# Kernel tuning notes

Hardware: AMD Instinct MI355X
Metric: run time of the kernel (lower is better)

Reference implementation:

```python
import jax, jax.numpy as jnp
import numpy as np

N_ACTOR = 128
NUM_MODS = 6
NUM_PTS = 30
N = 32768
B = 64
EPS = 1e-5


def _gn(x, g, b):
    # torch GroupNorm(1, C) on [..., C]: normalize over channel axis, affine
    m = jnp.mean(x, axis=-1, keepdims=True)
    v = jnp.mean((x - m) ** 2, axis=-1, keepdims=True)
    return (x - m) * jax.lax.rsqrt(v + EPS) * g + b


def setup_inputs() -> dict:
    key = jax.random.key(0)
    ks = jax.random.split(key, 32)
    d = N_ACTOR
    M = NUM_MODS
    s = 0.05
    rn = lambda k, shp: jax.random.normal(k, shp, jnp.float32) * s
    inp = {
        'actors': jax.random.normal(ks[0], (N, d), jnp.float32),
        'actor_ctrs': jax.random.normal(ks[1], (N, 2), jnp.float32),
        'actor_idcs': jnp.arange(N, dtype=jnp.int32).reshape(B, N // B),
        # per-mode residual MLP + output linear (stacked over modes)
        'pred_W1': rn(ks[2], (M, d, d)),
        'pred_g1': jnp.ones((M, d), jnp.float32),
        'pred_b1': jnp.zeros((M, d), jnp.float32),
        'pred_W2': rn(ks[3], (M, d, d)),
        'pred_g2': jnp.ones((M, d), jnp.float32),
        'pred_b2': jnp.zeros((M, d), jnp.float32),
        'pred_Wo': rn(ks[4], (M, d, 2 * NUM_PTS)),
        'pred_bo': rn(ks[5], (M, 2 * NUM_PTS)),
        # cls head: residual MLP + Linear(d,1)
        'cls_W1': rn(ks[6], (d, d)),
        'cls_g1': jnp.ones((d,), jnp.float32),
        'cls_b1': jnp.zeros((d,), jnp.float32),
        'cls_W2': rn(ks[7], (d, d)),
        'cls_g2': jnp.ones((d,), jnp.float32),
        'cls_b2': jnp.zeros((d,), jnp.float32),
        'cls_Wo': rn(ks[8], (d, 1)),
        'cls_bo': rn(ks[9], (1,)),
        # AttDest
        'att_dW1': rn(ks[10], (2, d)),
        'att_db1': rn(ks[11], (d,)),
        'att_dW2': rn(ks[12], (d, d)),
        'att_dg2': jnp.ones((d,), jnp.float32),
        'att_db2': jnp.zeros((d,), jnp.float32),
        'att_aW': rn(ks[13], (2 * d, d)),
        'att_ag': jnp.ones((d,), jnp.float32),
        'att_ab': jnp.zeros((d,), jnp.float32),
    }
    return inp


def reference(actors, actor_ctrs, actor_idcs, pred_W1, pred_g1, pred_b1,
              pred_W2, pred_g2, pred_b2, pred_Wo, pred_bo,
              cls_W1, cls_g1, cls_b1, cls_W2, cls_g2, cls_b2, cls_Wo, cls_bo,
              att_dW1, att_db1, att_dW2, att_dg2, att_db2,
              att_aW, att_ag, att_ab):
    n = actors.shape[0]
    M = pred_W1.shape[0]
    h = jnp.einsum('nc,mcd->mnd', actors, pred_W1)              # [M,N,d]
    h = jax.nn.relu(_gn(h, pred_g1[:, None, :], pred_b1[:, None, :]))
    h = _gn(jnp.einsum('mnd,mde->mne', h, pred_W2),
            pred_g2[:, None, :], pred_b2[:, None, :])
    h = jax.nn.relu(h + actors[None])                           # residual
    preds = jnp.einsum('mnd,mdo->mno', h, pred_Wo) + pred_bo[:, None, :]
    reg = preds.transpose(1, 0, 2).reshape(n, M, NUM_PTS, 2)    # [N,M,T,2]
    # per-scene reg[idcs] += ctrs: actor_idcs partitions arange(N), so this
    # is exactly a per-actor broadcast add of the (concatenated) centers
    reg = reg + actor_ctrs[:, None, None, :]
    dest_ctrs = jax.lax.stop_gradient(reg[:, :, -1, :])         # .detach()
    # --- AttDest ---
    dist = (actor_ctrs[:, None, :] - dest_ctrs).reshape(-1, 2)  # [N*M,2]
    dist = jax.nn.relu(dist @ att_dW1 + att_db1)
    dist = jax.nn.relu(_gn(dist @ att_dW2, att_dg2, att_db2))
    agts = jnp.broadcast_to(actors[:, None, :], (n, M, actors.shape[1]))
    agts = agts.reshape(-1, actors.shape[1])
    feats = jax.nn.relu(_gn(jnp.concatenate([dist, agts], axis=1) @ att_aW,
                            att_ag, att_ab))                    # [N*M,d]
    # --- cls head ---
    c = jax.nn.relu(_gn(feats @ cls_W1, cls_g1, cls_b1))
    c = _gn(c @ cls_W2, cls_g2, cls_b2)
    c = jax.nn.relu(c + feats)
    cls = (c @ cls_Wo + cls_bo).reshape(n, M)
    # --- sort modes by descending score, reorder reg accordingly ---
    order = jnp.argsort(-cls, axis=1)
    cls = jnp.take_along_axis(cls, order, axis=1)
    reg = jnp.take_along_axis(reg, order[:, :, None, None], axis=1)
    # train_model=True concatenates the per-scene splits back in order,
    # which reproduces the full arrays
    return cls, reg
```

## Files before the change

kernel.cpp:

```cpp
#include <hip/hip_runtime.h>

#define EPSV 1e-5f
#define CLS_SZ (32768*6)
#define FWS_FLOATS ((size_t)196608 * 128)

#define AL(ch,row) (((ch)<<7) + ((row) ^ ((((ch)&15))<<3)))

__device__ __forceinline__ float4 ld4(const float* p) { return *reinterpret_cast<const float4*>(p); }
__device__ __forceinline__ void st4(float* p, float4 v) { *reinterpret_cast<float4*>(p) = v; }

__device__ __forceinline__ void gemmA(const float* X, const float* __restrict__ Wg,
                                      float* WB0, float* WB1, float (&acc)[8][8],
                                      int ag, int jg4, int tid)
{
  float4 rA = ld4(Wg + tid*4);
  float4 rB = ld4(Wg + 1024 + tid*4);
  __syncthreads();
  st4(WB0 + tid*4, rA);
  st4(WB1 + tid*4, rB);
  __syncthreads();
  #pragma unroll 1
  for (int c = 0; c < 16; ++c) {
    float4 rN;
    const bool pf = (c + 2 < 16);
    if (pf) rN = ld4(Wg + (c+2)*1024 + tid*4);
    const float* WB = (c & 1) ? WB1 : WB0;
    #pragma unroll
    for (int kk = 0; kk < 8; ++kk) {
      int k = c*8 + kk;
      const float* xp = X + (k<<7) + ((ag<<3) ^ ((k & 15)<<3));
      float4 x0 = ld4(xp), x1 = ld4(xp + 4);
      float4 wl = ld4(WB + (kk<<7) + jg4);
      float4 wh = ld4(WB + (kk<<7) + 64 + jg4);
      float xv[8] = {x0.x,x0.y,x0.z,x0.w,x1.x,x1.y,x1.z,x1.w};
      float wv[8] = {wl.x,wl.y,wl.z,wl.w,wh.x,wh.y,wh.z,wh.w};
      #pragma unroll
      for (int r = 0; r < 8; ++r)
        #pragma unroll
        for (int c2 = 0; c2 < 8; ++c2)
          acc[r][c2] = fmaf(xv[r], wv[c2], acc[r][c2]);
    }
    __syncthreads();
    if (pf) st4(((c & 1) ? WB1 : WB0) + tid*4, rN);
  }
}

__device__ __forceinline__ void gemmWo(const float* X, const float* __restrict__ Wg,
                                       float* WB0, float* WB1, float (&acc)[8][4],
                                       int ag, int jg, int tid)
{
  const bool ld = tid < 120;
  const bool zp = (tid >= 120 && tid < 128);
  const int kk0 = ld ? (tid / 15) : (tid - 120);
  const int sl  = ld ? (tid % 15) * 4 : 60;
  float4 rA = {0,0,0,0}, rB = {0,0,0,0};
  if (ld) { rA = ld4(Wg + kk0*60 + sl); rB = ld4(Wg + 480 + kk0*60 + sl); }
  __syncthreads();
  if (ld || zp) { st4(WB0 + (kk0<<6) + sl, rA); st4(WB1 + (kk0<<6) + sl, rB); }
  __syncthreads();
  #pragma unroll 1
  for (int c = 0; c < 16; ++c) {
    float4 rN = {0,0,0,0};
    const bool pf = (c + 2 < 16);
    if (pf && ld) rN = ld4(Wg + (c+2)*480 + kk0*60 + sl);
    const float* WB = (c & 1) ? WB1 : WB0;
    #pragma unroll
    for (int kk = 0; kk < 8; ++kk) {
      int k = c*8 + kk;
      const float* xp = X + (k<<7) + ((ag<<3) ^ ((k & 15)<<3));
      float4 x0 = ld4(xp), x1 = ld4(xp + 4);
      float4 w = ld4(WB + (kk<<6) + jg*4);
      float xv[8] = {x0.x,x0.y,x0.z,x0.w,x1.x,x1.y,x1.z,x1.w};
      float wv[4] = {w.x,w.y,w.z,w.w};
      #pragma unroll
      for (int r = 0; r < 8; ++r)
        #pragma unroll
        for (int c2 = 0; c2 < 4; ++c2)
          acc[r][c2] = fmaf(xv[r], wv[c2], acc[r][c2]);
    }
    __syncthreads();
    if (pf && (ld || zp)) st4(((c & 1) ? WB1 : WB0) + (kk0<<6) + sl, rN);
  }
}

__device__ __forceinline__ void gn_finish(float* PS1, float* PS2, float* MEAN, float* RSTD, int tid)
{
  __syncthreads();
  if (tid < 128) {
    float a = 0.f, b = 0.f;
    #pragma unroll
    for (int j = 0; j < 4; ++j) { a += PS1[tid*4 + j]; b += PS2[tid*4 + j]; }
    float mu = a * 0.0078125f;
    float var = b * 0.0078125f - mu*mu;
    MEAN[tid] = mu;
    RSTD[tid] = rsqrtf(var + EPSV);
  }
  __syncthreads();
}

__device__ __forceinline__ void gn_reduce8(const float (&acc)[8][8], float* PS1, float* PS2,
                                           float* MEAN, float* RSTD, int ag, int jg, int tid)
{
  #pragma unroll
  for (int r = 0; r < 8; ++r) {
    float s = 0.f, q = 0.f;
    #pragma unroll
    for (int c = 0; c < 8; ++c) { float v = acc[r][c]; s += v; q += v*v; }
    s += __shfl_xor(s, 1, 64); q += __shfl_xor(q, 1, 64);
    s += __shfl_xor(s, 2, 64); q += __shfl_xor(q, 2, 64);
    if ((jg & 3) == 0) { int row = ag*8 + r; PS1[row*4 + (jg>>2)] = s; PS2[row*4 + (jg>>2)] = q; }
  }
  gn_finish(PS1, PS2, MEAN, RSTD, tid);
}

__global__ void __launch_bounds__(256, 2) pred_kernel(
    const float* __restrict__ actors, const float* __restrict__ ctrs,
    const float* __restrict__ W1, const float* __restrict__ g1v, const float* __restrict__ b1v,
    const float* __restrict__ W2, const float* __restrict__ g2v, const float* __restrict__ b2v,
    const float* __restrict__ Wo, const float* __restrict__ bov,
    float* __restrict__ out_reg)
{
  __shared__ __align__(16) float ACT[16384];
  __shared__ __align__(16) float WB0[1024], WB1[1024];
  __shared__ float MEAN[128], RSTD[128];
  float* PS1 = WB0;
  float* PS2 = WB1;

  const int tid = threadIdx.x;
  const int jg = tid & 15, ag = tid >> 4;
  const int jg4 = jg*4;
  const int m  = blockIdx.y;
  const int n0 = blockIdx.x * 128;

  #pragma unroll
  for (int p = 0; p < 16; ++p) {
    int i = (p<<8) + tid;
    int r = i >> 5, q4 = (i & 31) << 2;
    float4 v = ld4(actors + (size_t)(n0 + r)*128 + q4);
    ACT[AL(q4+0, r)] = v.x; ACT[AL(q4+1, r)] = v.y;
    ACT[AL(q4+2, r)] = v.z; ACT[AL(q4+3, r)] = v.w;
  }

  float acc[8][8];
  #pragma unroll
  for (int r = 0; r < 8; ++r)
    #pragma unroll
    for (int c = 0; c < 8; ++c) acc[r][c] = 0.f;

  gemmA(ACT, W1 + (size_t)m*16384, WB0, WB1, acc, ag, jg4, tid);
  gn_reduce8(acc, PS1, PS2, MEAN, RSTD, ag, jg, tid);
  {
    float mu[8], rs[8];
    #pragma unroll
    for (int r = 0; r < 8; ++r) { mu[r] = MEAN[ag*8+r]; rs[r] = RSTD[ag*8+r]; }
    float4 gl = ld4(g1v + m*128 + jg4), gh = ld4(g1v + m*128 + 64 + jg4);
    float4 bl = ld4(b1v + m*128 + jg4), bh = ld4(b1v + m*128 + 64 + jg4);
    float gv[8] = {gl.x,gl.y,gl.z,gl.w,gh.x,gh.y,gh.z,gh.w};
    float bv[8] = {bl.x,bl.y,bl.z,bl.w,bh.x,bh.y,bh.z,bh.w};
    float vm[8][8];
    #pragma unroll
    for (int r = 0; r < 8; ++r)
      #pragma unroll
      for (int c = 0; c < 8; ++c)
        vm[r][c] = fmaxf((acc[r][c] - mu[r]) * rs[r] * gv[c] + bv[c], 0.f);
    #pragma unroll
    for (int c = 0; c < 8; ++c) {
      int ch = (c < 4) ? (jg4 + c) : (64 + jg4 + (c - 4));
      int base = (ch<<7) + ((ag<<3) ^ ((ch & 15)<<3));
      st4(ACT + base,     make_float4(vm[0][c],vm[1][c],vm[2][c],vm[3][c]));
      st4(ACT + base + 4, make_float4(vm[4][c],vm[5][c],vm[6][c],vm[7][c]));
    }
  }

  #pragma unroll
  for (int r = 0; r < 8; ++r)
    #pragma unroll
    for (int c = 0; c < 8; ++c) acc[r][c] = 0.f;

  gemmA(ACT, W2 + (size_t)m*16384, WB0, WB1, acc, ag, jg4, tid);
  gn_reduce8(acc, PS1, PS2, MEAN, RSTD, ag, jg, tid);
  {
    float mu[8], rs[8];
    #pragma unroll
    for (int r = 0; r < 8; ++r) { mu[r] = MEAN[ag*8+r]; rs[r] = RSTD[ag*8+r]; }
    float4 gl = ld4(g2v + m*128 + jg4), gh = ld4(g2v + m*128 + 64 + jg4);
    float4 bl = ld4(b2v + m*128 + jg4), bh = ld4(b2v + m*128 + 64 + jg4);
    float gv[8] = {gl.x,gl.y,gl.z,gl.w,gh.x,gh.y,gh.z,gh.w};
    float bv[8] = {bl.x,bl.y,bl.z,bl.w,bh.x,bh.y,bh.z,bh.w};
    float vm[8][8];
    #pragma unroll
    for (int r = 0; r < 8; ++r) {
      const float* ap = actors + (size_t)(n0 + ag*8 + r)*128;
      float4 a0 = ld4(ap + jg4), a1 = ld4(ap + 64 + jg4);
      float av[8] = {a0.x,a0.y,a0.z,a0.w,a1.x,a1.y,a1.z,a1.w};
      #pragma unroll
      for (int c = 0; c < 8; ++c)
        vm[r][c] = fmaxf((acc[r][c] - mu[r]) * rs[r] * gv[c] + bv[c] + av[c], 0.f);
    }
    #pragma unroll
    for (int c = 0; c < 8; ++c) {
      int ch = (c < 4) ? (jg4 + c) : (64 + jg4 + (c - 4));
      int base = (ch<<7) + ((ag<<3) ^ ((ch & 15)<<3));
      st4(ACT + base,     make_float4(vm[0][c],vm[1][c],vm[2][c],vm[3][c]));
      st4(ACT + base + 4, make_float4(vm[4][c],vm[5][c],vm[6][c],vm[7][c]));
    }
  }

  float acc2[8][4];
  #pragma unroll
  for (int r = 0; r < 8; ++r)
    #pragma unroll
    for (int c = 0; c < 4; ++c) acc2[r][c] = 0.f;
  gemmWo(ACT, Wo + (size_t)m*7680, WB0, WB1, acc2, ag, jg, tid);

  if (jg < 15) {
    float4 bo4 = ld4(bov + m*60 + jg4);
    #pragma unroll
    for (int r = 0; r < 8; ++r) {
      int n = n0 + ag*8 + r;
      float2 cc = *reinterpret_cast<const float2*>(ctrs + 2*n);
      float4 v;
      v.x = acc2[r][0] + bo4.x + cc.x;
      v.y = acc2[r][1] + bo4.y + cc.y;
      v.z = acc2[r][2] + bo4.z + cc.x;
      v.w = acc2[r][3] + bo4.w + cc.y;
      st4(out_reg + (size_t)n*360 + m*60 + jg4, v);
    }
  }
}

__global__ void __launch_bounds__(256, 2) att_feats_kernel(
    const float* __restrict__ actors, const float* __restrict__ ctrs,
    const float* __restrict__ dW1, const float* __restrict__ db1,
    const float* __restrict__ dW2, const float* __restrict__ dg2, const float* __restrict__ db2,
    const float* __restrict__ aW, const float* __restrict__ aG, const float* __restrict__ aB,
    const float* __restrict__ reg, float* __restrict__ fws)
{
  __shared__ __align__(16) float ACT[16384];
  __shared__ __align__(16) float WB0[1024], WB1[1024];
  __shared__ float MEAN[128], RSTD[128];
  float* PS1 = WB0;
  float* PS2 = WB1;
  float* D0x = MEAN;
  float* D0y = RSTD;

  const int tid = threadIdx.x;
  const int jg = tid & 15, ag = tid >> 4;
  const int jg4 = jg*4;
  const int r0 = blockIdx.x * 128;

  if (tid < 128) {
    int rg = r0 + tid;
    int n = rg / 6, mm = rg - 6*n;
    size_t base = (size_t)n*360 + mm*60;
    float2 c2 = *reinterpret_cast<const float2*>(ctrs + 2*n);
    D0x[tid] = c2.x - reg[base + 58];
    D0y[tid] = c2.y - reg[base + 59];
  }
  __syncthreads();

  {
    float dx[8], dy[8];
    #pragma unroll
    for (int r = 0; r < 8; ++r) { dx[r] = D0x[ag*8+r]; dy[r] = D0y[ag*8+r]; }
    #pragma unroll
    for (int c = 0; c < 8; ++c) {
      int ch = (c < 4) ? (jg4 + c) : (64 + jg4 + (c - 4));
      float w1 = dW1[ch], w2 = dW1[128 + ch], bb = db1[ch];
      float v[8];
      #pragma unroll
      for (int r = 0; r < 8; ++r) v[r] = fmaxf(fmaf(dx[r], w1, fmaf(dy[r], w2, bb)), 0.f);
      int base = (ch<<7) + ((ag<<3) ^ ((ch & 15)<<3));
      st4(ACT + base,     make_float4(v[0],v[1],v[2],v[3]));
      st4(ACT + base + 4, make_float4(v[4],v[5],v[6],v[7]));
    }
  }

  float acc[8][8];
  #pragma unroll
  for (int r = 0; r < 8; ++r)
    #pragma unroll
    for (int c = 0; c < 8; ++c) acc[r][c] = 0.f;

  gemmA(ACT, dW2, WB0, WB1, acc, ag, jg4, tid);
  gn_reduce8(acc, PS1, PS2, MEAN, RSTD, ag, jg, tid);
  {
    float mu[8], rs[8];
    #pragma unroll
    for (int r = 0; r < 8; ++r) { mu[r] = MEAN[ag*8+r]; rs[r] = RSTD[ag*8+r]; }
    float4 gl = ld4(dg2 + jg4), gh = ld4(dg2 + 64 + jg4);
    float4 bl = ld4(db2 + jg4), bh = ld4(db2 + 64 + jg4);
    float gv[8] = {gl.x,gl.y,gl.z,gl.w,gh.x,gh.y,gh.z,gh.w};
    float bv[8] = {bl.x,bl.y,bl.z,bl.w,bh.x,bh.y,bh.z,bh.w};
    float vm[8][8];
    #pragma unroll
    for (int r = 0; r < 8; ++r)
      #pragma unroll
      for (int c = 0; c < 8; ++c)
        vm[r][c] = fmaxf((acc[r][c] - mu[r]) * rs[r] * gv[c] + bv[c], 0.f);
    #pragma unroll
    for (int c = 0; c < 8; ++c) {
      int ch = (c < 4) ? (jg4 + c) : (64 + jg4 + (c - 4));
      int base = (ch<<7) + ((ag<<3) ^ ((ch & 15)<<3));
      st4(ACT + base,     make_float4(vm[0][c],vm[1][c],vm[2][c],vm[3][c]));
      st4(ACT + base + 4, make_float4(vm[4][c],vm[5][c],vm[6][c],vm[7][c]));
    }
  }

  #pragma unroll
  for (int r = 0; r < 8; ++r)
    #pragma unroll
    for (int c = 0; c < 8; ++c) acc[r][c] = 0.f;
  gemmA(ACT, aW, WB0, WB1, acc, ag, jg4, tid);
  #pragma unroll
  for (int p = 0; p < 16; ++p) {
    int i = (p<<8) + tid;
    int r = i >> 5, q4 = (i & 31) << 2;
    int n = (r0 + r) / 6;
    float4 v = ld4(actors + (size_t)n*128 + q4);
    ACT[AL(q4+0, r)] = v.x; ACT[AL(q4+1, r)] = v.y;
    ACT[AL(q4+2, r)] = v.z; ACT[AL(q4+3, r)] = v.w;
  }
  gemmA(ACT, aW + 16384, WB0, WB1, acc, ag, jg4, tid);
  gn_reduce8(acc, PS1, PS2, MEAN, RSTD, ag, jg, tid);
  {
    float mu[8], rs[8];
    #pragma unroll
    for (int r = 0; r < 8; ++r) { mu[r] = MEAN[ag*8+r]; rs[r] = RSTD[ag*8+r]; }
    float4 gl = ld4(aG + jg4), gh = ld4(aG + 64 + jg4);
    float4 bl = ld4(aB + jg4), bh = ld4(aB + 64 + jg4);
    float gv[8] = {gl.x,gl.y,gl.z,gl.w,gh.x,gh.y,gh.z,gh.w};
    float bv[8] = {bl.x,bl.y,bl.z,bl.w,bh.x,bh.y,bh.z,bh.w};
    #pragma unroll
    for (int r = 0; r < 8; ++r) {
      float fv[8];
      #pragma unroll
      for (int c = 0; c < 8; ++c)
        fv[c] = fmaxf((acc[r][c] - mu[r]) * rs[r] * gv[c] + bv[c], 0.f);
      float* fp = fws + (size_t)(r0 + ag*8 + r)*128;
      st4(fp + jg4,      make_float4(fv[0],fv[1],fv[2],fv[3]));
      st4(fp + 64 + jg4, make_float4(fv[4],fv[5],fv[6],fv[7]));
    }
  }
}

__global__ void __launch_bounds__(256, 2) att_cls2_kernel(
    const float* __restrict__ cW1, const float* __restrict__ cg1, const float* __restrict__ cb1,
    const float* __restrict__ cW2, const float* __restrict__ cg2, const float* __restrict__ cb2,
    const float* __restrict__ cWo, const float* __restrict__ cbo,
    const float* __restrict__ fws, float* __restrict__ cls_out)
{
  __shared__ __align__(16) float ACT[16384];
  __shared__ __align__(16) float WB0[1024], WB1[1024];
  __shared__ float MEAN[128], RSTD[128];
  float* PS1 = WB0;
  float* PS2 = WB1;

  const int tid = threadIdx.x;
  const int jg = tid & 15, ag = tid >> 4;
  const int jg4 = jg*4;
  const int r0 = blockIdx.x * 128;

  #pragma unroll
  for (int p = 0; p < 16; ++p) {
    int i = (p<<8) + tid;
    int r = i >> 5, q4 = (i & 31) << 2;
    float4 v = ld4(fws + (size_t)(r0 + r)*128 + q4);
    ACT[AL(q4+0, r)] = v.x; ACT[AL(q4+1, r)] = v.y;
    ACT[AL(q4+2, r)] = v.z; ACT[AL(q4+3, r)] = v.w;
  }

  float acc[8][8];
  #pragma unroll
  for (int r = 0; r < 8; ++r)
    #pragma unroll
    for (int c = 0; c < 8; ++c) acc[r][c] = 0.f;

  gemmA(ACT, cW1, WB0, WB1, acc, ag, jg4, tid);
  gn_reduce8(acc, PS1, PS2, MEAN, RSTD, ag, jg, tid);
  {
    float mu[8], rs[8];
    #pragma unroll
    for (int r = 0; r < 8; ++r) { mu[r] = MEAN[ag*8+r]; rs[r] = RSTD[ag*8+r]; }
    float4 gl = ld4(cg1 + jg4), gh = ld4(cg1 + 64 + jg4);
    float4 bl = ld4(cb1 + jg4), bh = ld4(cb1 + 64 + jg4);
    float gv[8] = {gl.x,gl.y,gl.z,gl.w,gh.x,gh.y,gh.z,gh.w};
    float bv[8] = {bl.x,bl.y,bl.z,bl.w,bh.x,bh.y,bh.z,bh.w};
    float vm[8][8];
    #pragma unroll
    for (int r = 0; r < 8; ++r)
      #pragma unroll
      for (int c = 0; c < 8; ++c)
        vm[r][c] = fmaxf((acc[r][c] - mu[r]) * rs[r] * gv[c] + bv[c], 0.f);
    #pragma unroll
    for (int c = 0; c < 8; ++c) {
      int ch = (c < 4) ? (jg4 + c) : (64 + jg4 + (c - 4));
      int base = (ch<<7) + ((ag<<3) ^ ((ch & 15)<<3));
      st4(ACT + base,     make_float4(vm[0][c],vm[1][c],vm[2][c],vm[3][c]));
      st4(ACT + base + 4, make_float4(vm[4][c],vm[5][c],vm[6][c],vm[7][c]));
    }
  }

  #pragma unroll
  for (int r = 0; r < 8; ++r)
    #pragma unroll
    for (int c = 0; c < 8; ++c) acc[r][c] = 0.f;
  gemmA(ACT, cW2, WB0, WB1, acc, ag, jg4, tid);
  gn_reduce8(acc, PS1, PS2, MEAN, RSTD, ag, jg, tid);
  {
    float mu[8], rs[8];
    #pragma unroll
    for (int r = 0; r < 8; ++r) { mu[r] = MEAN[ag*8+r]; rs[r] = RSTD[ag*8+r]; }
    float4 gl = ld4(cg2 + jg4), gh = ld4(cg2 + 64 + jg4);
    float4 bl = ld4(cb2 + jg4), bh = ld4(cb2 + 64 + jg4);
    float4 wl = ld4(cWo + jg4), wh = ld4(cWo + 64 + jg4);
    float gv[8] = {gl.x,gl.y,gl.z,gl.w,gh.x,gh.y,gh.z,gh.w};
    float bv[8] = {bl.x,bl.y,bl.z,bl.w,bh.x,bh.y,bh.z,bh.w};
    float wv[8] = {wl.x,wl.y,wl.z,wl.w,wh.x,wh.y,wh.z,wh.w};
    #pragma unroll
    for (int r = 0; r < 8; ++r) {
      const float* fp = fws + (size_t)(r0 + ag*8 + r)*128;
      float4 a0 = ld4(fp + jg4), a1 = ld4(fp + 64 + jg4);
      float av[8] = {a0.x,a0.y,a0.z,a0.w,a1.x,a1.y,a1.z,a1.w};
      float p = 0.f;
      #pragma unroll
      for (int c = 0; c < 8; ++c) {
        float v = (acc[r][c] - mu[r]) * rs[r] * gv[c] + bv[c];
        v = fmaxf(v + av[c], 0.f);
        p = fmaf(v, wv[c], p);
      }
      float s = p;
      s += __shfl_xor(s, 1, 64);
      s += __shfl_xor(s, 2, 64);
      if ((jg & 3) == 0) PS1[(ag*8+r)*4 + (jg>>2)] = s;
    }
  }
  __syncthreads();
  if (tid < 128) {
    float s = 0.f;
    #pragma unroll
    for (int j = 0; j < 4; ++j) s += PS1[tid*4 + j];
    cls_out[r0 + tid] = s + cbo[0];
  }
}

__global__ void __launch_bounds__(256, 2) att_cls_mono_kernel(
    const float* __restrict__ actors, const float* __restrict__ ctrs,
    const float* __restrict__ dW1, const float* __restrict__ db1,
    const float* __restrict__ dW2, const float* __restrict__ dg2, const float* __restrict__ db2,
    const float* __restrict__ aW, const float* __restrict__ aG, const float* __restrict__ aB,
    const float* __restrict__ cW1, const float* __restrict__ cg1, const float* __restrict__ cb1,
    const float* __restrict__ cW2, const float* __restrict__ cg2, const float* __restrict__ cb2,
    const float* __restrict__ cWo, const float* __restrict__ cbo,
    const float* __restrict__ reg, float* __restrict__ cls_out)
{
  __shared__ __align__(16) float ACT[16384];
  __shared__ __align__(16) float WB0[1024], WB1[1024];
  __shared__ float MEAN[128], RSTD[128];
  float* PS1 = WB0;
  float* PS2 = WB1;
  float* D0x = MEAN;
  float* D0y = RSTD;

  const int tid = threadIdx.x;
  const int jg = tid & 15, ag = tid >> 4;
  const int jg4 = jg*4;
  const int r0 = blockIdx.x * 128;

  if (tid < 128) {
    int rg = r0 + tid;
    int n = rg / 6, mm = rg - 6*n;
    size_t base = (size_t)n*360 + mm*60;
    float2 c2 = *reinterpret_cast<const float2*>(ctrs + 2*n);
    D0x[tid] = c2.x - reg[base + 58];
    D0y[tid] = c2.y - reg[base + 59];
  }
  __syncthreads();

  {
    float dx[8], dy[8];
    #pragma unroll
    for (int r = 0; r < 8; ++r) { dx[r] = D0x[ag*8+r]; dy[r] = D0y[ag*8+r]; }
    #pragma unroll
    for (int c = 0; c < 8; ++c) {
      int ch = (c < 4) ? (jg4 + c) : (64 + jg4 + (c - 4));
      float w1 = dW1[ch], w2 = dW1[128 + ch], bb = db1[ch];
      float v[8];
      #pragma unroll
      for (int r = 0; r < 8; ++r) v[r] = fmaxf(fmaf(dx[r], w1, fmaf(dy[r], w2, bb)), 0.f);
      int base = (ch<<7) + ((ag<<3) ^ ((ch & 15)<<3));
      st4(ACT + base,     make_float4(v[0],v[1],v[2],v[3]));
      st4(ACT + base + 4, make_float4(v[4],v[5],v[6],v[7]));
    }
  }

  float acc[8][8];
  #pragma unroll
  for (int r = 0; r < 8; ++r)
    #pragma unroll
    for (int c = 0; c < 8; ++c) acc[r][c] = 0.f;

  gemmA(ACT, dW2, WB0, WB1, acc, ag, jg4, tid);
  gn_reduce8(acc, PS1, PS2, MEAN, RSTD, ag, jg, tid);
  {
    float mu[8], rs[8];
    #pragma unroll
    for (int r = 0; r < 8; ++r) { mu[r] = MEAN[ag*8+r]; rs[r] = RSTD[ag*8+r]; }
    float4 gl = ld4(dg2 + jg4), gh = ld4(dg2 + 64 + jg4);
    float4 bl = ld4(db2 + jg4), bh = ld4(db2 + 64 + jg4);
    float gv[8] = {gl.x,gl.y,gl.z,gl.w,gh.x,gh.y,gh.z,gh.w};
    float bv[8] = {bl.x,bl.y,bl.z,bl.w,bh.x,bh.y,bh.z,bh.w};
    float vm[8][8];
    #pragma unroll
    for (int r = 0; r < 8; ++r)
      #pragma unroll
      for (int c = 0; c < 8; ++c)
        vm[r][c] = fmaxf((acc[r][c] - mu[r]) * rs[r] * gv[c] + bv[c], 0.f);
    #pragma unroll
    for (int c = 0; c < 8; ++c) {
      int ch = (c < 4) ? (jg4 + c) : (64 + jg4 + (c - 4));
      int base = (ch<<7) + ((ag<<3) ^ ((ch & 15)<<3));
      st4(ACT + base,     make_float4(vm[0][c],vm[1][c],vm[2][c],vm[3][c]));
      st4(ACT + base + 4, make_float4(vm[4][c],vm[5][c],vm[6][c],vm[7][c]));
    }
  }

  #pragma unroll
  for (int r = 0; r < 8; ++r)
    #pragma unroll
    for (int c = 0; c < 8; ++c) acc[r][c] = 0.f;
  gemmA(ACT, aW, WB0, WB1, acc, ag, jg4, tid);
  #pragma unroll
  for (int p = 0; p < 16; ++p) {
    int i = (p<<8) + tid;
    int r = i >> 5, q4 = (i & 31) << 2;
    int n = (r0 + r) / 6;
    float4 v = ld4(actors + (size_t)n*128 + q4);
    ACT[AL(q4+0, r)] = v.x; ACT[AL(q4+1, r)] = v.y;
    ACT[AL(q4+2, r)] = v.z; ACT[AL(q4+3, r)] = v.w;
  }
  gemmA(ACT, aW + 16384, WB0, WB1, acc, ag, jg4, tid);
  gn_reduce8(acc, PS1, PS2, MEAN, RSTD, ag, jg, tid);
  float feats[8][8];
  {
    float mu[8], rs[8];
    #pragma unroll
    for (int r = 0; r < 8; ++r) { mu[r] = MEAN[ag*8+r]; rs[r] = RSTD[ag*8+r]; }
    float4 gl = ld4(aG + jg4), gh = ld4(aG + 64 + jg4);
    float4 bl = ld4(aB + jg4), bh = ld4(aB + 64 + jg4);
    float gv[8] = {gl.x,gl.y,gl.z,gl.w,gh.x,gh.y,gh.z,gh.w};
    float bv[8] = {bl.x,bl.y,bl.z,bl.w,bh.x,bh.y,bh.z,bh.w};
    #pragma unroll
    for (int r = 0; r < 8; ++r)
      #pragma unroll
      for (int c = 0; c < 8; ++c)
        feats[r][c] = fmaxf((acc[r][c] - mu[r]) * rs[r] * gv[c] + bv[c], 0.f);
    #pragma unroll
    for (int c = 0; c < 8; ++c) {
      int ch = (c < 4) ? (jg4 + c) : (64 + jg4 + (c - 4));
      int base = (ch<<7) + ((ag<<3) ^ ((ch & 15)<<3));
      st4(ACT + base,     make_float4(feats[0][c],feats[1][c],feats[2][c],feats[3][c]));
      st4(ACT + base + 4, make_float4(feats[4][c],feats[5][c],feats[6][c],feats[7][c]));
    }
  }

  #pragma unroll
  for (int r = 0; r < 8; ++r)
    #pragma unroll
    for (int c = 0; c < 8; ++c) acc[r][c] = 0.f;
  gemmA(ACT, cW1, WB0, WB1, acc, ag, jg4, tid);
  gn_reduce8(acc, PS1, PS2, MEAN, RSTD, ag, jg, tid);
  {
    float mu[8], rs[8];
    #pragma unroll
    for (int r = 0; r < 8; ++r) { mu[r] = MEAN[ag*8+r]; rs[r] = RSTD[ag*8+r]; }
    float4 gl = ld4(cg1 + jg4), gh = ld4(cg1 + 64 + jg4);
    float4 bl = ld4(cb1 + jg4), bh = ld4(cb1 + 64 + jg4);
    float gv[8] = {gl.x,gl.y,gl.z,gl.w,gh.x,gh.y,gh.z,gh.w};
    float bv[8] = {bl.x,bl.y,bl.z,bl.w,bh.x,bh.y,bh.z,bh.w};
    float vm[8][8];
    #pragma unroll
    for (int r = 0; r < 8; ++r)
      #pragma unroll
      for (int c = 0; c < 8; ++c)
        vm[r][c] = fmaxf((acc[r][c] - mu[r]) * rs[r] * gv[c] + bv[c], 0.f);
    #pragma unroll
    for (int c = 0; c < 8; ++c) {
      int ch = (c < 4) ? (jg4 + c) : (64 + jg4 + (c - 4));
      int base = (ch<<7) + ((ag<<3) ^ ((ch & 15)<<3));
      st4(ACT + base,     make_float4(vm[0][c],vm[1][c],vm[2][c],vm[3][c]));
      st4(ACT + base + 4, make_float4(vm[4][c],vm[5][c],vm[6][c],vm[7][c]));
    }
  }

  #pragma unroll
  for (int r = 0; r < 8; ++r)
    #pragma unroll
    for (int c = 0; c < 8; ++c) acc[r][c] = 0.f;
  gemmA(ACT, cW2, WB0, WB1, acc, ag, jg4, tid);
  gn_reduce8(acc, PS1, PS2, MEAN, RSTD, ag, jg, tid);
  {
    float mu[8], rs[8], p[8];
    #pragma unroll
    for (int r = 0; r < 8; ++r) { mu[r] = MEAN[ag*8+r]; rs[r] = RSTD[ag*8+r]; p[r] = 0.f; }
    float4 gl = ld4(cg2 + jg4), gh = ld4(cg2 + 64 + jg4);
    float4 bl = ld4(cb2 + jg4), bh = ld4(cb2 + 64 + jg4);
    float4 wl = ld4(cWo + jg4), wh = ld4(cWo + 64 + jg4);
    float gv[8] = {gl.x,gl.y,gl.z,gl.w,gh.x,gh.y,gh.z,gh.w};
    float bv[8] = {bl.x,bl.y,bl.z,bl.w,bh.x,bh.y,bh.z,bh.w};
    float wv[8] = {wl.x,wl.y,wl.z,wl.w,wh.x,wh.y,wh.z,wh.w};
    #pragma unroll
    for (int c = 0; c < 8; ++c) {
      #pragma unroll
      for (int r = 0; r < 8; ++r) {
        float v = (acc[r][c] - mu[r]) * rs[r] * gv[c] + bv[c];
        v = fmaxf(v + feats[r][c], 0.f);
        p[r] = fmaf(v, wv[c], p[r]);
      }
    }
    #pragma unroll
    for (int r = 0; r < 8; ++r) {
      float s = p[r];
      s += __shfl_xor(s, 1, 64);
      s += __shfl_xor(s, 2, 64);
      if ((jg & 3) == 0) PS1[(ag*8+r)*4 + (jg>>2)] = s;
    }
  }
  __syncthreads();
  if (tid < 128) {
    float s = 0.f;
    #pragma unroll
    for (int j = 0; j < 4; ++j) s += PS1[tid*4 + j];
    cls_out[r0 + tid] = s + cbo[0];
  }
}

__global__ void __launch_bounds__(256) sort_kernel(float* __restrict__ out)
{
  __shared__ float RL[64*360];
  __shared__ float CL[64*6];
  __shared__ float CS[64*6];
  __shared__ int   ORD[64*6];

  const int tid = threadIdx.x;
  const int n0 = blockIdx.x * 64;
  float* regp = out + CLS_SZ;

  for (int i = tid; i < 64*360; i += 256) RL[i] = regp[(size_t)n0*360 + i];
  for (int i = tid; i < 384; i += 256)    CL[i] = out[n0*6 + i];
  __syncthreads();

  if (tid < 64) {
    float v[6];
    #pragma unroll
    for (int m2 = 0; m2 < 6; ++m2) v[m2] = CL[tid*6 + m2];
    int used = 0;
    for (int j = 0; j < 6; ++j) {
      int best = -1; float bv = 0.f;
      for (int m2 = 0; m2 < 6; ++m2) {
        if (used & (1 << m2)) continue;
        if (best < 0 || v[m2] > bv) { best = m2; bv = v[m2]; }
      }
      used |= (1 << best);
      ORD[tid*6 + j] = best;
      CS[tid*6 + j] = bv;
    }
  }
  __syncthreads();

  for (int i = tid; i < 384; i += 256) out[n0*6 + i] = CS[i];
  for (int i = tid; i < 64*360; i += 256) {
    int rl = i / 360, rem = i - rl*360;
    int slot = rem / 60, j = rem - slot*60;
    out[CLS_SZ + (size_t)n0*360 + i] = RL[rl*360 + ORD[rl*6 + slot]*60 + j];
  }
}

extern "C" void kernel_launch(void* const* d_in, const int* in_sizes, int n_in,
                              void* d_out, int out_size, void* d_ws, size_t ws_size,
                              hipStream_t stream)
{
  (void)in_sizes; (void)n_in; (void)out_size;
  const float* actors = (const float*)d_in[0];
  const float* ctrs   = (const float*)d_in[1];
  const float* pW1 = (const float*)d_in[3];
  const float* pg1 = (const float*)d_in[4];
  const float* pb1 = (const float*)d_in[5];
  const float* pW2 = (const float*)d_in[6];
  const float* pg2 = (const float*)d_in[7];
  const float* pb2 = (const float*)d_in[8];
  const float* pWo = (const float*)d_in[9];
  const float* pbo = (const float*)d_in[10];
  const float* cW1 = (const float*)d_in[11];
  const float* cg1 = (const float*)d_in[12];
  const float* cb1 = (const float*)d_in[13];
  const float* cW2 = (const float*)d_in[14];
  const float* cg2 = (const float*)d_in[15];
  const float* cb2 = (const float*)d_in[16];
  const float* cWo = (const float*)d_in[17];
  const float* cbo = (const float*)d_in[18];
  const float* dW1 = (const float*)d_in[19];
  const float* db1 = (const float*)d_in[20];
  const float* dW2 = (const float*)d_in[21];
  const float* dg2 = (const float*)d_in[22];
  const float* db2 = (const float*)d_in[23];
  const float* aW  = (const float*)d_in[24];
  const float* aG  = (const float*)d_in[25];
  const float* aB  = (const float*)d_in[26];

  float* out = (float*)d_out;
  float* out_reg = out + CLS_SZ;
  float* fws = (float*)d_ws;
  const bool split = ws_size >= FWS_FLOATS * sizeof(float);

  dim3 gA(256, 6);
  pred_kernel<<<gA, 256, 0, stream>>>(actors, ctrs, pW1, pg1, pb1, pW2, pg2, pb2,
                                      pWo, pbo, out_reg);
  if (split) {
    att_feats_kernel<<<1536, 256, 0, stream>>>(actors, ctrs,
                                               dW1, db1, dW2, dg2, db2,
                                               aW, aG, aB, out_reg, fws);
    att_cls2_kernel<<<1536, 256, 0, stream>>>(cW1, cg1, cb1, cW2, cg2, cb2,
                                              cWo, cbo, fws, out);
  } else {
    att_cls_mono_kernel<<<1536, 256, 0, stream>>>(actors, ctrs,
                                                  dW1, db1, dW2, dg2, db2,
                                                  aW, aG, aB,
                                                  cW1, cg1, cb1, cW2, cg2, cb2, cWo, cbo,
                                                  out_reg, out);
  }
  sort_kernel<<<512, 256, 0, stream>>>(out);
}
```

Baseline: 767.9 us.

## Load GEMM weights straight from global into registers instead of staging through LDS

The shared-memory double-buffered weight staging in the GEMM helpers is replaced with per-thread register double-buffered loads of weight rows from global memory (L2/L1 cached), which removes the per-chunk __syncthreads and the LDS weight traffic. Explicit barriers are added around activation-tile rewrites, and the GroupNorm partial-sum buffers become dedicated shared arrays. Each thread now issues many small redundant global loads of the same weights, so performance depends on cache hit rates and load latency hiding, and register pressure rises.

```diff
diff --git a/kernel.cpp b/kernel.cpp
--- a/kernel.cpp
+++ b/kernel.cpp
@@ -9,77 +9,88 @@
 __device__ __forceinline__ float4 ld4(const float* p) { return *reinterpret_cast<const float4*>(p); }
 __device__ __forceinline__ void st4(float* p, float4 v) { *reinterpret_cast<float4*>(p) = v; }
 
-__device__ __forceinline__ void gemmA(const float* X, const float* __restrict__ Wg,
-                                      float* WB0, float* WB1, float (&acc)[8][8],
-                                      int ag, int jg4, int tid)
-{
-  float4 rA = ld4(Wg + tid*4);
-  float4 rB = ld4(Wg + 1024 + tid*4);
-  __syncthreads();
-  st4(WB0 + tid*4, rA);
-  st4(WB1 + tid*4, rB);
-  __syncthreads();
+__device__ __forceinline__ void ldW2(const float* __restrict__ Wg, int k0, int jg4,
+                                     float4 (&w0)[2], float4 (&w1)[2])
+{
+  #pragma unroll
+  for (int kk = 0; kk < 2; ++kk) {
+    w0[kk] = ld4(Wg + (k0 + kk)*128 + jg4);
+    w1[kk] = ld4(Wg + (k0 + kk)*128 + 64 + jg4);
+  }
+}
+
+__device__ __forceinline__ void fma2(const float* X, int k0, int ag,
+                                     const float4 (&w0)[2], const float4 (&w1)[2],
+                                     float (&acc)[8][8])
+{
+  #pragma unroll
+  for (int kk = 0; kk < 2; ++kk) {
+    int k = k0 + kk;
+    const float* xp = X + (k<<7) + ((ag<<3) ^ ((k & 15)<<3));
+    float4 x0 = ld4(xp), x1 = ld4(xp + 4);
+    float xv[8] = {x0.x,x0.y,x0.z,x0.w,x1.x,x1.y,x1.z,x1.w};
+    float wv[8] = {w0[kk].x,w0[kk].y,w0[kk].z,w0[kk].w,
+                   w1[kk].x,w1[kk].y,w1[kk].z,w1[kk].w};
+    #pragma unroll
+    for (int r = 0; r < 8; ++r)
+      #pragma unroll
+      for (int c2 = 0; c2 < 8; ++c2)
+        acc[r][c2] = fmaf(xv[r], wv[c2], acc[r][c2]);
+  }
+}
+
+__device__ __forceinline__ void gemmR(const float* X, const float* __restrict__ Wg,
+                                      float (&acc)[8][8], int ag, int jg4)
+{
+  float4 a0[2], a1[2], b0[2], b1[2];
+  ldW2(Wg, 0, jg4, a0, a1);
   #pragma unroll 1
-  for (int c = 0; c < 16; ++c) {
-    float4 rN;
-    const bool pf = (c + 2 < 16);
-    if (pf) rN = ld4(Wg + (c+2)*1024 + tid*4);
-    const float* WB = (c & 1) ? WB1 : WB0;
-    #pragma unroll
-    for (int kk = 0; kk < 8; ++kk) {
-      int k = c*8 + kk;
-      const float* xp = X + (k<<7) + ((ag<<3) ^ ((k & 15)<<3));
-      float4 x0 = ld4(xp), x1 = ld4(xp + 4);
-      float4 wl = ld4(WB + (kk<<7) + jg4);
-      float4 wh = ld4(WB + (kk<<7) + 64 + jg4);
-      float xv[8] = {x0.x,x0.y,x0.z,x0.w,x1.x,x1.y,x1.z,x1.w};
-      float wv[8] = {wl.x,wl.y,wl.z,wl.w,wh.x,wh.y,wh.z,wh.w};
-      #pragma unroll
-      for (int r = 0; r < 8; ++r)
-        #pragma unroll
-        for (int c2 = 0; c2 < 8; ++c2)
-          acc[r][c2] = fmaf(xv[r], wv[c2], acc[r][c2]);
-    }
-    __syncthreads();
-    if (pf) st4(((c & 1) ? WB1 : WB0) + tid*4, rN);
-  }
-}
-
-__device__ __forceinline__ void gemmWo(const float* X, const float* __restrict__ Wg,
-                                       float* WB0, float* WB1, float (&acc)[8][4],
-                                       int ag, int jg, int tid)
-{
-  const bool ld = tid < 120;
-  const bool zp = (tid >= 120 && tid < 128);
-  const int kk0 = ld ? (tid / 15) : (tid - 120);
-  const int sl  = ld ? (tid % 15) * 4 : 60;
-  float4 rA = {0,0,0,0}, rB = {0,0,0,0};
-  if (ld) { rA = ld4(Wg + kk0*60 + sl); rB = ld4(Wg + 480 + kk0*60 + sl); }
-  __syncthreads();
-  if (ld || zp) { st4(WB0 + (kk0<<6) + sl, rA); st4(WB1 + (kk0<<6) + sl, rB); }
-  __syncthreads();
+  for (int c = 0; c < 64; c += 2) {
+    ldW2(Wg, (c+1)*2, jg4, b0, b1);
+    fma2(X, c*2, ag, a0, a1, acc);
+    if (c + 2 < 64) ldW2(Wg, (c+2)*2, jg4, a0, a1);
+    fma2(X, (c+1)*2, ag, b0, b1, acc);
+  }
+}
+
+__device__ __forceinline__ void ldWo(const float* __restrict__ Wg, int k0, int jg,
+                                     bool ldw, float4 (&w)[8])
+{
+  #pragma unroll
+  for (int kk = 0; kk < 8; ++kk)
+    w[kk] = ldw ? ld4(Wg + (k0 + kk)*60 + jg*4) : make_float4(0.f,0.f,0.f,0.f);
+}
+
+__device__ __forceinline__ void fmaWo(const float* X, int k0, int ag,
+                                      const float4 (&w)[8], float (&acc)[8][4])
+{
+  #pragma unroll
+  for (int kk = 0; kk < 8; ++kk) {
+    int k = k0 + kk;
+    const float* xp = X + (k<<7) + ((ag<<3) ^ ((k & 15)<<3));
+    float4 x0 = ld4(xp), x1 = ld4(xp + 4);
+    float xv[8] = {x0.x,x0.y,x0.z,x0.w,x1.x,x1.y,x1.z,x1.w};
+    float wv[4] = {w[kk].x,w[kk].y,w[kk].z,w[kk].w};
+    #pragma unroll
+    for (int r = 0; r < 8; ++r)
+      #pragma unroll
+      for (int c2 = 0; c2 < 4; ++c2)
+        acc[r][c2] = fmaf(xv[r], wv[c2], acc[r][c2]);
+  }
+}
+
+__device__ __forceinline__ void gemmWoR(const float* X, const float* __restrict__ Wg,
+                                        float (&acc)[8][4], int ag, int jg)
+{
+  const bool ldw = (jg < 15);
+  float4 a[8], b[8];
+  ldWo(Wg, 0, jg, ldw, a);
   #pragma unroll 1
-  for (int c = 0; c < 16; ++c) {
-    float4 rN = {0,0,0,0};
-    const bool pf = (c + 2 < 16);
-    if (pf && ld) rN = ld4(Wg + (c+2)*480 + kk0*60 + sl);
-    const float* WB = (c & 1) ? WB1 : WB0;
-    #pragma unroll
-    for (int kk = 0; kk < 8; ++kk) {
-      int k = c*8 + kk;
-      const float* xp = X + (k<<7) + ((ag<<3) ^ ((k & 15)<<3));
-      float4 x0 = ld4(xp), x1 = ld4(xp + 4);
-      float4 w = ld4(WB + (kk<<6) + jg*4);
-      float xv[8] = {x0.x,x0.y,x0.z,x0.w,x1.x,x1.y,x1.z,x1.w};
-      float wv[4] = {w.x,w.y,w.z,w.w};
-      #pragma unroll
-      for (int r = 0; r < 8; ++r)
-        #pragma unroll
-        for (int c2 = 0; c2 < 4; ++c2)
-          acc[r][c2] = fmaf(xv[r], wv[c2], acc[r][c2]);
-    }
-    __syncthreads();
-    if (pf && (ld || zp)) st4(((c & 1) ? WB1 : WB0) + (kk0<<6) + sl, rN);
+  for (int c = 0; c < 16; c += 2) {
+    ldWo(Wg, (c+1)*8, jg, ldw, b);
+    fmaWo(X, c*8, ag, a, acc);
+    if (c + 2 < 16) ldWo(Wg, (c+2)*8, jg, ldw, a);
+    fmaWo(X, (c+1)*8, ag, b, acc);
   }
 }
 
@@ -121,10 +132,7 @@
     float* __restrict__ out_reg)
 {
   __shared__ __align__(16) float ACT[16384];
-  __shared__ __align__(16) float WB0[1024], WB1[1024];
-  __shared__ float MEAN[128], RSTD[128];
-  float* PS1 = WB0;
-  float* PS2 = WB1;
+  __shared__ float PS1[512], PS2[512], MEAN[128], RSTD[128];
 
   const int tid = threadIdx.x;
   const int jg = tid & 15, ag = tid >> 4;
@@ -140,6 +148,7 @@
     ACT[AL(q4+0, r)] = v.x; ACT[AL(q4+1, r)] = v.y;
     ACT[AL(q4+2, r)] = v.z; ACT[AL(q4+3, r)] = v.w;
   }
+  __syncthreads();
 
   float acc[8][8];
   #pragma unroll
@@ -147,7 +156,7 @@
     #pragma unroll
     for (int c = 0; c < 8; ++c) acc[r][c] = 0.f;
 
-  gemmA(ACT, W1 + (size_t)m*16384, WB0, WB1, acc, ag, jg4, tid);
+  gemmR(ACT, W1 + (size_t)m*16384, acc, ag, jg4);
   gn_reduce8(acc, PS1, PS2, MEAN, RSTD, ag, jg, tid);
   {
     float mu[8], rs[8];
@@ -171,13 +180,14 @@
       st4(ACT + base + 4, make_float4(vm[4][c],vm[5][c],vm[6][c],vm[7][c]));
     }
   }
-
-  #pragma unroll
-  for (int r = 0; r < 8; ++r)
-    #pragma unroll
-    for (int c = 0; c < 8; ++c) acc[r][c] = 0.f;
-
-  gemmA(ACT, W2 + (size_t)m*16384, WB0, WB1, acc, ag, jg4, tid);
+  __syncthreads();
+
+  #pragma unroll
+  for (int r = 0; r < 8; ++r)
+    #pragma unroll
+    for (int c = 0; c < 8; ++c) acc[r][c] = 0.f;
+
+  gemmR(ACT, W2 + (size_t)m*16384, acc, ag, jg4);
   gn_reduce8(acc, PS1, PS2, MEAN, RSTD, ag, jg, tid);
   {
     float mu[8], rs[8];
@@ -205,13 +215,14 @@
       st4(ACT + base + 4, make_float4(vm[4][c],vm[5][c],vm[6][c],vm[7][c]));
     }
   }
+  __syncthreads();
 
   float acc2[8][4];
   #pragma unroll
   for (int r = 0; r < 8; ++r)
     #pragma unroll
     for (int c = 0; c < 4; ++c) acc2[r][c] = 0.f;
-  gemmWo(ACT, Wo + (size_t)m*7680, WB0, WB1, acc2, ag, jg, tid);
+  gemmWoR(ACT, Wo + (size_t)m*7680, acc2, ag, jg);
 
   if (jg < 15) {
     float4 bo4 = ld4(bov + m*60 + jg4);
@@ -237,10 +248,7 @@
     const float* __restrict__ reg, float* __restrict__ fws)
 {
   __shared__ __align__(16) float ACT[16384];
-  __shared__ __align__(16) float WB0[1024], WB1[1024];
-  __shared__ float MEAN[128], RSTD[128];
-  float* PS1 = WB0;
-  float* PS2 = WB1;
+  __shared__ float PS1[512], PS2[512], MEAN[128], RSTD[128];
   float* D0x = MEAN;
   float* D0y = RSTD;
 
@@ -275,6 +283,7 @@
       st4(ACT + base + 4, make_float4(v[4],v[5],v[6],v[7]));
     }
   }
+  __syncthreads();
 
   float acc[8][8];
   #pragma unroll
@@ -282,7 +291,7 @@
     #pragma unroll
     for (int c = 0; c < 8; ++c) acc[r][c] = 0.f;
 
-  gemmA(ACT, dW2, WB0, WB1, acc, ag, jg4, tid);
+  gemmR(ACT, dW2, acc, ag, jg4);
   gn_reduce8(acc, PS1, PS2, MEAN, RSTD, ag, jg, tid);
   {
     float mu[8], rs[8];
@@ -306,12 +315,14 @@
       st4(ACT + base + 4, make_float4(vm[4][c],vm[5][c],vm[6][c],vm[7][c]));
     }
   }
-
-  #pragma unroll
-  for (int r = 0; r < 8; ++r)
-    #pragma unroll
-    for (int c = 0; c < 8; ++c) acc[r][c] = 0.f;
-  gemmA(ACT, aW, WB0, WB1, acc, ag, jg4, tid);
+  __syncthreads();
+
+  #pragma unroll
+  for (int r = 0; r < 8; ++r)
+    #pragma unroll
+    for (int c = 0; c < 8; ++c) acc[r][c] = 0.f;
+  gemmR(ACT, aW, acc, ag, jg4);
+  __syncthreads();
   #pragma unroll
   for (int p = 0; p < 16; ++p) {
     int i = (p<<8) + tid;
@@ -321,7 +332,8 @@
     ACT[AL(q4+0, r)] = v.x; ACT[AL(q4+1, r)] = v.y;
     ACT[AL(q4+2, r)] = v.z; ACT[AL(q4+3, r)] = v.w;
   }
-  gemmA(ACT, aW + 16384, WB0, WB1, acc, ag, jg4, tid);
+  __syncthreads();
+  gemmR(ACT, aW + 16384, acc, ag, jg4);
   gn_reduce8(acc, PS1, PS2, MEAN, RSTD, ag, jg, tid);
   {
     float mu[8], rs[8];
@@ -351,10 +363,7 @@
     const float* __restrict__ fws, float* __restrict__ cls_out)
 {
   __shared__ __align__(16) float ACT[16384];
-  __shared__ __align__(16) float WB0[1024], WB1[1024];
-  __shared__ float MEAN[128], RSTD[128];
-  float* PS1 = WB0;
-  float* PS2 = WB1;
+  __shared__ float PS1[512], PS2[512], MEAN[128], RSTD[128];
 
   const int tid = threadIdx.x;
   const int jg = tid & 15, ag = tid >> 4;
@@ -369,6 +378,7 @@
     ACT[AL(q4+0, r)] = v.x; ACT[AL(q4+1, r)] = v.y;
     ACT[AL(q4+2, r)] = v.z; ACT[AL(q4+3, r)] = v.w;
   }
+  __syncthreads();
 
   float acc[8][8];
   #pragma unroll
@@ -376,7 +386,7 @@
     #pragma unroll
     for (int c = 0; c < 8; ++c) acc[r][c] = 0.f;
 
-  gemmA(ACT, cW1, WB0, WB1, acc, ag, jg4, tid);
+  gemmR(ACT, cW1, acc, ag, jg4);
   gn_reduce8(acc, PS1, PS2, MEAN, RSTD, ag, jg, tid);
   {
     float mu[8], rs[8];
@@ -400,12 +410,13 @@
       st4(ACT + base + 4, make_float4(vm[4][c],vm[5][c],vm[6][c],vm[7][c]));
     }
   }
-
-  #pragma unroll
-  for (int r = 0; r < 8; ++r)
-    #pragma unroll
-    for (int c = 0; c < 8; ++c) acc[r][c] = 0.f;
-  gemmA(ACT, cW2, WB0, WB1, acc, ag, jg4, tid);
+  __syncthreads();
+
+  #pragma unroll
+  for (int r = 0; r < 8; ++r)
+    #pragma unroll
+    for (int c = 0; c < 8; ++c) acc[r][c] = 0.f;
+  gemmR(ACT, cW2, acc, ag, jg4);
   gn_reduce8(acc, PS1, PS2, MEAN, RSTD, ag, jg, tid);
   {
     float mu[8], rs[8];
@@ -455,10 +466,7 @@
     const float* __restrict__ reg, float* __restrict__ cls_out)
 {
   __shared__ __align__(16) float ACT[16384];
-  __shared__ __align__(16) float WB0[1024], WB1[1024];
-  __shared__ float MEAN[128], RSTD[128];
-  float* PS1 = WB0;
-  float* PS2 = WB1;
+  __shared__ float PS1[512], PS2[512], MEAN[128], RSTD[128];
   float* D0x = MEAN;
   float* D0y = RSTD;
 
@@ -493,6 +501,7 @@
       st4(ACT + base + 4, make_float4(v[4],v[5],v[6],v[7]));
     }
   }
+  __syncthreads();
 
   float acc[8][8];
   #pragma unroll
@@ -500,7 +509,7 @@
     #pragma unroll
     for (int c = 0; c < 8; ++c) acc[r][c] = 0.f;
 
-  gemmA(ACT, dW2, WB0, WB1, acc, ag, jg4, tid);
+  gemmR(ACT, dW2, acc, ag, jg4);
   gn_reduce8(acc, PS1, PS2, MEAN, RSTD, ag, jg, tid);
   {
     float mu[8], rs[8];
@@ -524,12 +533,14 @@
       st4(ACT + base + 4, make_float4(vm[4][c],vm[5][c],vm[6][c],vm[7][c]));
     }
   }
-
-  #pragma unroll
-  for (int r = 0; r < 8; ++r)
-    #pragma unroll
-    for (int c = 0; c < 8; ++c) acc[r][c] = 0.f;
-  gemmA(ACT, aW, WB0, WB1, acc, ag, jg4, tid);
+  __syncthreads();
+
+  #pragma unroll
+  for (int r = 0; r < 8; ++r)
+    #pragma unroll
+    for (int c = 0; c < 8; ++c) acc[r][c] = 0.f;
+  gemmR(ACT, aW, acc, ag, jg4);
+  __syncthreads();
   #pragma unroll
   for (int p = 0; p < 16; ++p) {
     int i = (p<<8) + tid;
@@ -539,7 +550,8 @@
     ACT[AL(q4+0, r)] = v.x; ACT[AL(q4+1, r)] = v.y;
     ACT[AL(q4+2, r)] = v.z; ACT[AL(q4+3, r)] = v.w;
   }
-  gemmA(ACT, aW + 16384, WB0, WB1, acc, ag, jg4, tid);
+  __syncthreads();
+  gemmR(ACT, aW + 16384, acc, ag, jg4);
   gn_reduce8(acc, PS1, PS2, MEAN, RSTD, ag, jg, tid);
   float feats[8][8];
   {
@@ -563,12 +575,13 @@
       st4(ACT + base + 4, make_float4(feats[4][c],feats[5][c],feats[6][c],feats[7][c]));
     }
   }
-
-  #pragma unroll
-  for (int r = 0; r < 8; ++r)
-    #pragma unroll
-    for (int c = 0; c < 8; ++c) acc[r][c] = 0.f;
-  gemmA(ACT, cW1, WB0, WB1, acc, ag, jg4, tid);
+  __syncthreads();
+
+  #pragma unroll
+  for (int r = 0; r < 8; ++r)
+    #pragma unroll
+    for (int c = 0; c < 8; ++c) acc[r][c] = 0.f;
+  gemmR(ACT, cW1, acc, ag, jg4);
   gn_reduce8(acc, PS1, PS2, MEAN, RSTD, ag, jg, tid);
   {
     float mu[8], rs[8];
@@ -592,12 +605,13 @@
       st4(ACT + base + 4, make_float4(vm[4][c],vm[5][c],vm[6][c],vm[7][c]));
     }
   }
-
-  #pragma unroll
-  for (int r = 0; r < 8; ++r)
-    #pragma unroll
-    for (int c = 0; c < 8; ++c) acc[r][c] = 0.f;
-  gemmA(ACT, cW2, WB0, WB1, acc, ag, jg4, tid);
+  __syncthreads();
+
+  #pragma unroll
+  for (int r = 0; r < 8; ++r)
+    #pragma unroll
+    for (int c = 0; c < 8; ++c) acc[r][c] = 0.f;
+  gemmR(ACT, cW2, acc, ag, jg4);
   gn_reduce8(acc, PS1, PS2, MEAN, RSTD, ag, jg, tid);
   {
     float mu[8], rs[8], p[8];
```

After: 789.9 us. +2.9%, slower.
